# Kernel tuning notes

Measured on AMD Instinct MI355X. Metric: run time of the kernel, lower is better.

The kernel has to match this reference:

```python
import jax, jax.numpy as jnp
import numpy as np

B = 2048
INPUT_SIZE = 40960
HIDDEN = 256
ACTIVE = 30  # ~active features per chess position


def _multi_hot(key):
    idx = jax.random.randint(key, (B, ACTIVE), 0, INPUT_SIZE)
    oh = jnp.zeros((B, INPUT_SIZE), jnp.float32)
    return oh.at[jnp.arange(B)[:, None], idx].set(1.0)


def setup_inputs() -> dict:
    key = jax.random.key(0)
    kw, kb, ks, k1, k2, k3, k4 = jax.random.split(key, 7)
    white_onehot = _multi_hot(kw)
    black_onehot = _multi_hot(kb)
    stm = jax.random.randint(ks, (B, 1), 0, 2).astype(jnp.float32)
    # parameters (PyTorch Linear layout: weight [out, in])
    ft_w = jax.random.normal(k1, (HIDDEN, INPUT_SIZE), jnp.float32) * 0.02
    ft_b = jnp.zeros((HIDDEN,), jnp.float32)
    l1_w = jax.random.normal(k2, (32, HIDDEN * 2), jnp.float32) * 0.05
    l1_b = jnp.zeros((32,), jnp.float32)
    l2_w = jax.random.normal(k3, (32, 32), jnp.float32) * 0.1
    l2_b = jnp.zeros((32,), jnp.float32)
    l3_w = jax.random.normal(k4, (1, 32), jnp.float32) * 0.1
    l3_b = jnp.zeros((1,), jnp.float32)
    return dict(white_onehot=white_onehot, black_onehot=black_onehot, stm=stm,
                ft_w=ft_w, ft_b=ft_b, l1_w=l1_w, l1_b=l1_b,
                l2_w=l2_w, l2_b=l2_b, l3_w=l3_w, l3_b=l3_b)


def reference(white_onehot, black_onehot, stm,
              ft_w, ft_b, l1_w, l1_b, l2_w, l2_b, l3_w, l3_b):
    # feature transformer applied to dense one-hots (the wasteful dense GEMM)
    wh = jnp.clip(white_onehot @ ft_w.T + ft_b, 0.0, 1.0)  # [B, H]
    bh = jnp.clip(black_onehot @ ft_w.T + ft_b, 0.0, 1.0)  # [B, H]
    # side-to-move dependent perspective ordering
    hidden = jnp.where(stm.astype(bool),
                       jnp.concatenate([wh, bh], axis=-1),
                       jnp.concatenate([bh, wh], axis=-1))  # [B, 2H]
    x = jnp.clip(hidden @ l1_w.T + l1_b, 0.0, 1.0)
    x = jnp.clip(x @ l2_w.T + l2_b, 0.0, 1.0)
    return x @ l3_w.T + l3_b  # [B, 1]
```

## Files before the change

### kernel.cpp

```cpp
#include <hip/hip_runtime.h>

#define BATCH 2048
#define IN_SZ 40960
#define IN4   (IN_SZ / 4)
#define HID   256
#define LCAP  64

__global__ __launch_bounds__(256) void ft_transpose(const float* __restrict__ ftw,
                                                    float* __restrict__ ftT) {
    __shared__ float tile[32][33];
    const int tx = threadIdx.x;
    const int ty = threadIdx.y;
    const int bx = blockIdx.x;
    const int by = blockIdx.y;

    const int col = bx * 32 + tx;
#pragma unroll
    for (int j = 0; j < 32; j += 8) {
        const int row = by * 32 + ty + j;
        tile[ty + j][tx] = ftw[(size_t)row * IN_SZ + col];
    }
    __syncthreads();

    const int ocol = by * 32 + tx;
#pragma unroll
    for (int j = 0; j < 32; j += 8) {
        const int orow = bx * 32 + ty + j;
        ftT[(size_t)orow * HID + ocol] = tile[tx][ty + j];
    }
}

__global__ __launch_bounds__(256) void extract(const float* __restrict__ wo,
                                               const float* __restrict__ bo,
                                               int* __restrict__ cnt,
                                               int* __restrict__ lists)
{
    const int persp = blockIdx.y;
    const float4* __restrict__ src = (const float4*)(persp ? bo : wo);
    const int stride = gridDim.x * blockDim.x;
    for (int i = blockIdx.x * blockDim.x + threadIdx.x; i < BATCH * IN4; i += stride) {
        const float4 v = src[i];
        if (((v.x + v.y) + (v.z + v.w)) != 0.f) {
            const int row = i / IN4;
            const int f0  = (i - row * IN4) * 4;
            int* c = cnt + row * 2 + persp;
            int* l = lists + (row * 2 + persp) * LCAP;
            if (v.x != 0.f) l[atomicAdd(c, 1)] = f0;
            if (v.y != 0.f) l[atomicAdd(c, 1)] = f0 + 1;
            if (v.z != 0.f) l[atomicAdd(c, 1)] = f0 + 2;
            if (v.w != 0.f) l[atomicAdd(c, 1)] = f0 + 3;
        }
    }
}

__global__ __launch_bounds__(256) void ft_mlp(
    const int* __restrict__ cnt, const int* __restrict__ lists,
    const float* __restrict__ stm,
    const float* __restrict__ ftT, const float* __restrict__ ftb,
    const float* __restrict__ l1w, const float* __restrict__ l1b,
    const float* __restrict__ l2w, const float* __restrict__ l2b,
    const float* __restrict__ l3w, const float* __restrict__ l3b,
    float* __restrict__ out) {
    __shared__ int   sidx[2 * LCAP];
    __shared__ float hidden[2 * HID];
    __shared__ float x1[32], x2[32];

    const int b = blockIdx.x;
    const int t = threadIdx.x;

    if (t < 2 * LCAP) sidx[t] = lists[b * 2 * LCAP + t];
    __syncthreads();

    const int cw = cnt[b * 2 + 0];
    const int cb = cnt[b * 2 + 1];

    float accw = ftb[t];
    float accb = accw;
    for (int j = 0; j < cw; ++j) accw += ftT[(size_t)sidx[j] * HID + t];
    for (int j = 0; j < cb; ++j) accb += ftT[(size_t)sidx[LCAP + j] * HID + t];
    accw = fminf(fmaxf(accw, 0.f), 1.f);
    accb = fminf(fmaxf(accb, 0.f), 1.f);

    const bool s = (stm[b] != 0.f);
    hidden[t]       = s ? accw : accb;
    hidden[HID + t] = s ? accb : accw;
    __syncthreads();

    {
        const int o = t >> 3;
        const int part = t & 7;
        const float* w1 = l1w + o * (2 * HID);
        float sum = 0.f;
#pragma unroll 8
        for (int i = part; i < 2 * HID; i += 8)
            sum += hidden[i] * w1[i];
        sum += __shfl_xor(sum, 1);
        sum += __shfl_xor(sum, 2);
        sum += __shfl_xor(sum, 4);
        if (part == 0) x1[o] = fminf(fmaxf(sum + l1b[o], 0.f), 1.f);
    }
    __syncthreads();

    if (t < 32) {
        const float* w2 = l2w + t * 32;
        float sum = l2b[t];
#pragma unroll
        for (int i = 0; i < 32; ++i) sum += x1[i] * w2[i];
        x2[t] = fminf(fmaxf(sum, 0.f), 1.f);
    }
    __syncthreads();

    if (t == 0) {
        float sum = l3b[0];
#pragma unroll
        for (int i = 0; i < 32; ++i) sum += x2[i] * l3w[i];
        out[b] = sum;
    }
}

__global__ __launch_bounds__(256) void nnue_fused_fallback(
    const float* __restrict__ wo, const float* __restrict__ bo,
    const float* __restrict__ stm,
    const float* __restrict__ ftw, const float* __restrict__ ftb,
    const float* __restrict__ l1w, const float* __restrict__ l1b,
    const float* __restrict__ l2w, const float* __restrict__ l2b,
    const float* __restrict__ l3w, const float* __restrict__ l3b,
    float* __restrict__ out) {
    __shared__ int   idxw[LCAP], idxb[LCAP];
    __shared__ int   cntw, cntb;
    __shared__ float hidden[2 * HID];
    __shared__ float x1[32], x2[32];

    const int b = blockIdx.x;
    const int t = threadIdx.x;
    if (t == 0) { cntw = 0; cntb = 0; }
    __syncthreads();

    const float4* wrow = (const float4*)(wo + (size_t)b * IN_SZ);
    const float4* brow = (const float4*)(bo + (size_t)b * IN_SZ);
    for (int i = t; i < IN4; i += 256) {
        float4 v = wrow[i];
        float4 u = brow[i];
        if (((v.x + v.y) + (v.z + v.w)) != 0.f) {
            if (v.x != 0.f) idxw[atomicAdd(&cntw, 1)] = 4 * i;
            if (v.y != 0.f) idxw[atomicAdd(&cntw, 1)] = 4 * i + 1;
            if (v.z != 0.f) idxw[atomicAdd(&cntw, 1)] = 4 * i + 2;
            if (v.w != 0.f) idxw[atomicAdd(&cntw, 1)] = 4 * i + 3;
        }
        if (((u.x + u.y) + (u.z + u.w)) != 0.f) {
            if (u.x != 0.f) idxb[atomicAdd(&cntb, 1)] = 4 * i;
            if (u.y != 0.f) idxb[atomicAdd(&cntb, 1)] = 4 * i + 1;
            if (u.z != 0.f) idxb[atomicAdd(&cntb, 1)] = 4 * i + 2;
            if (u.w != 0.f) idxb[atomicAdd(&cntb, 1)] = 4 * i + 3;
        }
    }
    __syncthreads();

    float accw = ftb[t], accb = accw;
    for (int j = 0; j < cntw; ++j) accw += ftw[(size_t)t * IN_SZ + idxw[j]];
    for (int j = 0; j < cntb; ++j) accb += ftw[(size_t)t * IN_SZ + idxb[j]];
    accw = fminf(fmaxf(accw, 0.f), 1.f);
    accb = fminf(fmaxf(accb, 0.f), 1.f);

    const bool s = (stm[b] != 0.f);
    hidden[t]       = s ? accw : accb;
    hidden[HID + t] = s ? accb : accw;
    __syncthreads();

    {
        const int o = t >> 3, part = t & 7;
        const float* w1 = l1w + o * (2 * HID);
        float sum = 0.f;
        for (int i = part; i < 2 * HID; i += 8) sum += hidden[i] * w1[i];
        sum += __shfl_xor(sum, 1);
        sum += __shfl_xor(sum, 2);
        sum += __shfl_xor(sum, 4);
        if (part == 0) x1[o] = fminf(fmaxf(sum + l1b[o], 0.f), 1.f);
    }
    __syncthreads();
    if (t < 32) {
        float sum = l2b[t];
        for (int i = 0; i < 32; ++i) sum += x1[i] * l2w[t * 32 + i];
        x2[t] = fminf(fmaxf(sum, 0.f), 1.f);
    }
    __syncthreads();
    if (t == 0) {
        float sum = l3b[0];
        for (int i = 0; i < 32; ++i) sum += x2[i] * l3w[i];
        out[b] = sum;
    }
}

extern "C" void kernel_launch(void* const* d_in, const int* in_sizes, int n_in,
                              void* d_out, int out_size, void* d_ws, size_t ws_size,
                              hipStream_t stream) {
    const float* wo  = (const float*)d_in[0];
    const float* bo  = (const float*)d_in[1];
    const float* stm = (const float*)d_in[2];
    const float* ftw = (const float*)d_in[3];
    const float* ftb = (const float*)d_in[4];
    const float* l1w = (const float*)d_in[5];
    const float* l1b = (const float*)d_in[6];
    const float* l2w = (const float*)d_in[7];
    const float* l2b = (const float*)d_in[8];
    const float* l3w = (const float*)d_in[9];
    const float* l3b = (const float*)d_in[10];
    float* out = (float*)d_out;

    const size_t ftT_bytes  = (size_t)IN_SZ * HID * sizeof(float);
    const size_t cnt_off    = 44 * 1024 * 1024;
    const size_t cnt_bytes  = (size_t)BATCH * 2 * sizeof(int);
    const size_t list_off   = cnt_off + cnt_bytes;
    const size_t list_bytes = (size_t)BATCH * 2 * LCAP * sizeof(int);
    const size_t need       = list_off + list_bytes;

    if (ws_size >= need && ftT_bytes <= cnt_off) {
        float* ftT  = (float*)d_ws;
        int* cnt    = (int*)((char*)d_ws + cnt_off);
        int* lists  = (int*)((char*)d_ws + list_off);

        hipMemsetAsync(cnt, 0, cnt_bytes, stream);
        ft_transpose<<<dim3(IN_SZ / 32, HID / 32), dim3(32, 8), 0, stream>>>(ftw, ftT);
        extract<<<dim3(1024, 2), 256, 0, stream>>>(wo, bo, cnt, lists);
        ft_mlp<<<BATCH, 256, 0, stream>>>(cnt, lists, stm, ftT, ftb,
                                          l1w, l1b, l2w, l2b, l3w, l3b, out);
    } else {
        nnue_fused_fallback<<<BATCH, 256, 0, stream>>>(wo, bo, stm, ftw, ftb,
                                                       l1w, l1b, l2w, l2b, l3w, l3b, out);
    }
}
```

Before: 702.1 us.

## Fuse transpose, sparse extraction and MLP into one cooperative kernel

Replaces the memset plus three separate launches with a single cooperative kernel of 1024 blocks. Each block first transposes its share of the feature-transformer weights, then scans two batch rows' one-hot inputs and builds their index lists in shared memory, hits a grid-wide sync, and then runs the sparse accumulate and MLP for those rows. This removes launch gaps and the global count and list round-trip. In exchange it adds a grid barrier and needs 4 blocks per CU to be co-resident. Each block also handles two rows serially instead of one, which halves parallelism in the MLP phase.

Result: slower. 844.7 us (+20.3%).

```diff
diff --git a/kernel.cpp b/kernel.cpp
--- a/kernel.cpp
+++ b/kernel.cpp
@@ -1,120 +1,145 @@
 #include <hip/hip_runtime.h>
-
-#define BATCH 2048
-#define IN_SZ 40960
-#define IN4   (IN_SZ / 4)
-#define HID   256
-#define LCAP  64
-
-__global__ __launch_bounds__(256) void ft_transpose(const float* __restrict__ ftw,
-                                                    float* __restrict__ ftT) {
-    __shared__ float tile[32][33];
-    const int tx = threadIdx.x;
-    const int ty = threadIdx.y;
-    const int bx = blockIdx.x;
-    const int by = blockIdx.y;
-
-    const int col = bx * 32 + tx;
-#pragma unroll
-    for (int j = 0; j < 32; j += 8) {
-        const int row = by * 32 + ty + j;
-        tile[ty + j][tx] = ftw[(size_t)row * IN_SZ + col];
-    }
-    __syncthreads();
-
-    const int ocol = by * 32 + tx;
-#pragma unroll
-    for (int j = 0; j < 32; j += 8) {
-        const int orow = bx * 32 + ty + j;
-        ftT[(size_t)orow * HID + ocol] = tile[tx][ty + j];
-    }
-}
-
-__global__ __launch_bounds__(256) void extract(const float* __restrict__ wo,
-                                               const float* __restrict__ bo,
-                                               int* __restrict__ cnt,
-                                               int* __restrict__ lists)
-{
-    const int persp = blockIdx.y;
-    const float4* __restrict__ src = (const float4*)(persp ? bo : wo);
-    const int stride = gridDim.x * blockDim.x;
-    for (int i = blockIdx.x * blockDim.x + threadIdx.x; i < BATCH * IN4; i += stride) {
-        const float4 v = src[i];
-        if (((v.x + v.y) + (v.z + v.w)) != 0.f) {
-            const int row = i / IN4;
-            const int f0  = (i - row * IN4) * 4;
-            int* c = cnt + row * 2 + persp;
-            int* l = lists + (row * 2 + persp) * LCAP;
-            if (v.x != 0.f) l[atomicAdd(c, 1)] = f0;
-            if (v.y != 0.f) l[atomicAdd(c, 1)] = f0 + 1;
-            if (v.z != 0.f) l[atomicAdd(c, 1)] = f0 + 2;
-            if (v.w != 0.f) l[atomicAdd(c, 1)] = f0 + 3;
-        }
-    }
-}
-
-__global__ __launch_bounds__(256) void ft_mlp(
-    const int* __restrict__ cnt, const int* __restrict__ lists,
+#include <hip/hip_cooperative_groups.h>
+
+namespace cg = cooperative_groups;
+
+#define BATCH   2048
+#define IN_SZ   40960
+#define IN4     (IN_SZ / 4)
+#define HID     256
+#define LCAP    64
+#define NB      1024
+#define ROWS_PB (BATCH / NB)
+#define NTILES  ((IN_SZ / 32) * (HID / 32))
+
+__global__ __launch_bounds__(256, 4) void nnue_one(
+    const float* __restrict__ wo, const float* __restrict__ bo,
     const float* __restrict__ stm,
-    const float* __restrict__ ftT, const float* __restrict__ ftb,
+    const float* __restrict__ ftw, const float* __restrict__ ftb,
     const float* __restrict__ l1w, const float* __restrict__ l1b,
     const float* __restrict__ l2w, const float* __restrict__ l2b,
     const float* __restrict__ l3w, const float* __restrict__ l3b,
-    float* __restrict__ out) {
-    __shared__ int   sidx[2 * LCAP];
+    float* __restrict__ ftT, float* __restrict__ out)
+{
+    __shared__ float tile[32][33];
+    __shared__ int   idx[ROWS_PB][2][LCAP];
+    __shared__ int   cnt[ROWS_PB][2];
     __shared__ float hidden[2 * HID];
     __shared__ float x1[32], x2[32];
 
-    const int b = blockIdx.x;
-    const int t = threadIdx.x;
-
-    if (t < 2 * LCAP) sidx[t] = lists[b * 2 * LCAP + t];
-    __syncthreads();
-
-    const int cw = cnt[b * 2 + 0];
-    const int cb = cnt[b * 2 + 1];
-
-    float accw = ftb[t];
-    float accb = accw;
-    for (int j = 0; j < cw; ++j) accw += ftT[(size_t)sidx[j] * HID + t];
-    for (int j = 0; j < cb; ++j) accb += ftT[(size_t)sidx[LCAP + j] * HID + t];
-    accw = fminf(fmaxf(accw, 0.f), 1.f);
-    accb = fminf(fmaxf(accb, 0.f), 1.f);
-
-    const bool s = (stm[b] != 0.f);
-    hidden[t]       = s ? accw : accb;
-    hidden[HID + t] = s ? accb : accw;
-    __syncthreads();
+    const int t   = threadIdx.x;
+    const int blk = blockIdx.x;
+
+    if (t < ROWS_PB * 2) ((int*)cnt)[t] = 0;
 
     {
-        const int o = t >> 3;
-        const int part = t & 7;
-        const float* w1 = l1w + o * (2 * HID);
-        float sum = 0.f;
+        const int tx = t & 31;
+        const int ty = t >> 5;
+        for (int tid = blk; tid < NTILES; tid += NB) {
+            const int bx = tid >> 3;
+            const int by = tid & 7;
+            __syncthreads();
+#pragma unroll
+            for (int j = 0; j < 32; j += 8)
+                tile[ty + j][tx] = ftw[(size_t)(by * 32 + ty + j) * IN_SZ + bx * 32 + tx];
+            __syncthreads();
+#pragma unroll
+            for (int j = 0; j < 32; j += 8)
+                ftT[(size_t)(bx * 32 + ty + j) * HID + by * 32 + tx] = tile[tx][ty + j];
+        }
+    }
+    __syncthreads();
+
+    {
+        const int row0 = blk * ROWS_PB;
+        const float4* __restrict__ w0 = (const float4*)(wo + (size_t)row0 * IN_SZ);
+        const float4* __restrict__ b0 = (const float4*)(bo + (size_t)row0 * IN_SZ);
+        const float4* __restrict__ w1 = (const float4*)(wo + (size_t)(row0 + 1) * IN_SZ);
+        const float4* __restrict__ b1 = (const float4*)(bo + (size_t)(row0 + 1) * IN_SZ);
+
+        for (int i = t; i < IN4; i += 256) {
+            const float4 a0 = w0[i];
+            const float4 a1 = b0[i];
+            const float4 a2 = w1[i];
+            const float4 a3 = b1[i];
+            const int f0 = 4 * i;
+            if (((a0.x + a0.y) + (a0.z + a0.w)) != 0.f) {
+                if (a0.x != 0.f) idx[0][0][atomicAdd(&cnt[0][0], 1)] = f0;
+                if (a0.y != 0.f) idx[0][0][atomicAdd(&cnt[0][0], 1)] = f0 + 1;
+                if (a0.z != 0.f) idx[0][0][atomicAdd(&cnt[0][0], 1)] = f0 + 2;
+                if (a0.w != 0.f) idx[0][0][atomicAdd(&cnt[0][0], 1)] = f0 + 3;
+            }
+            if (((a1.x + a1.y) + (a1.z + a1.w)) != 0.f) {
+                if (a1.x != 0.f) idx[0][1][atomicAdd(&cnt[0][1], 1)] = f0;
+                if (a1.y != 0.f) idx[0][1][atomicAdd(&cnt[0][1], 1)] = f0 + 1;
+                if (a1.z != 0.f) idx[0][1][atomicAdd(&cnt[0][1], 1)] = f0 + 2;
+                if (a1.w != 0.f) idx[0][1][atomicAdd(&cnt[0][1], 1)] = f0 + 3;
+            }
+            if (((a2.x + a2.y) + (a2.z + a2.w)) != 0.f) {
+                if (a2.x != 0.f) idx[1][0][atomicAdd(&cnt[1][0], 1)] = f0;
+                if (a2.y != 0.f) idx[1][0][atomicAdd(&cnt[1][0], 1)] = f0 + 1;
+                if (a2.z != 0.f) idx[1][0][atomicAdd(&cnt[1][0], 1)] = f0 + 2;
+                if (a2.w != 0.f) idx[1][0][atomicAdd(&cnt[1][0], 1)] = f0 + 3;
+            }
+            if (((a3.x + a3.y) + (a3.z + a3.w)) != 0.f) {
+                if (a3.x != 0.f) idx[1][1][atomicAdd(&cnt[1][1], 1)] = f0;
+                if (a3.y != 0.f) idx[1][1][atomicAdd(&cnt[1][1], 1)] = f0 + 1;
+                if (a3.z != 0.f) idx[1][1][atomicAdd(&cnt[1][1], 1)] = f0 + 2;
+                if (a3.w != 0.f) idx[1][1][atomicAdd(&cnt[1][1], 1)] = f0 + 3;
+            }
+        }
+    }
+
+    cg::this_grid().sync();
+
+    for (int r = 0; r < ROWS_PB; ++r) {
+        const int row = blk * ROWS_PB + r;
+        const int cw = cnt[r][0];
+        const int cb = cnt[r][1];
+
+        float accw = ftb[t];
+        float accb = accw;
+        for (int j = 0; j < cw; ++j) accw += ftT[(size_t)idx[r][0][j] * HID + t];
+        for (int j = 0; j < cb; ++j) accb += ftT[(size_t)idx[r][1][j] * HID + t];
+        accw = fminf(fmaxf(accw, 0.f), 1.f);
+        accb = fminf(fmaxf(accb, 0.f), 1.f);
+
+        const bool s = (stm[row] != 0.f);
+        hidden[t]       = s ? accw : accb;
+        hidden[HID + t] = s ? accb : accw;
+        __syncthreads();
+
+        {
+            const int o = t >> 3;
+            const int part = t & 7;
+            const float* w1p = l1w + o * (2 * HID);
+            float sum = 0.f;
 #pragma unroll 8
-        for (int i = part; i < 2 * HID; i += 8)
-            sum += hidden[i] * w1[i];
-        sum += __shfl_xor(sum, 1);
-        sum += __shfl_xor(sum, 2);
-        sum += __shfl_xor(sum, 4);
-        if (part == 0) x1[o] = fminf(fmaxf(sum + l1b[o], 0.f), 1.f);
-    }
-    __syncthreads();
-
-    if (t < 32) {
-        const float* w2 = l2w + t * 32;
-        float sum = l2b[t];
-#pragma unroll
-        for (int i = 0; i < 32; ++i) sum += x1[i] * w2[i];
-        x2[t] = fminf(fmaxf(sum, 0.f), 1.f);
-    }
-    __syncthreads();
-
-    if (t == 0) {
-        float sum = l3b[0];
-#pragma unroll
-        for (int i = 0; i < 32; ++i) sum += x2[i] * l3w[i];
-        out[b] = sum;
+            for (int i = part; i < 2 * HID; i += 8)
+                sum += hidden[i] * w1p[i];
+            sum += __shfl_xor(sum, 1);
+            sum += __shfl_xor(sum, 2);
+            sum += __shfl_xor(sum, 4);
+            if (part == 0) x1[o] = fminf(fmaxf(sum + l1b[o], 0.f), 1.f);
+        }
+        __syncthreads();
+
+        if (t < 32) {
+            const float* w2 = l2w + t * 32;
+            float sum = l2b[t];
+#pragma unroll
+            for (int i = 0; i < 32; ++i) sum += x1[i] * w2[i];
+            x2[t] = fminf(fmaxf(sum, 0.f), 1.f);
+        }
+        __syncthreads();
+
+        if (t == 0) {
+            float sum = l3b[0];
+#pragma unroll
+            for (int i = 0; i < 32; ++i) sum += x2[i] * l3w[i];
+            out[row] = sum;
+        }
+        __syncthreads();
     }
 }
 
@@ -169,9 +194,9 @@
 
     {
         const int o = t >> 3, part = t & 7;
-        const float* w1 = l1w + o * (2 * HID);
+        const float* w1p = l1w + o * (2 * HID);
         float sum = 0.f;
-        for (int i = part; i < 2 * HID; i += 8) sum += hidden[i] * w1[i];
+        for (int i = part; i < 2 * HID; i += 8) sum += hidden[i] * w1p[i];
         sum += __shfl_xor(sum, 1);
         sum += __shfl_xor(sum, 2);
         sum += __shfl_xor(sum, 4);
@@ -207,24 +232,18 @@
     const float* l3b = (const float*)d_in[10];
     float* out = (float*)d_out;
 
-    const size_t ftT_bytes  = (size_t)IN_SZ * HID * sizeof(float);
-    const size_t cnt_off    = 44 * 1024 * 1024;
-    const size_t cnt_bytes  = (size_t)BATCH * 2 * sizeof(int);
-    const size_t list_off   = cnt_off + cnt_bytes;
-    const size_t list_bytes = (size_t)BATCH * 2 * LCAP * sizeof(int);
-    const size_t need       = list_off + list_bytes;
-
-    if (ws_size >= need && ftT_bytes <= cnt_off) {
-        float* ftT  = (float*)d_ws;
-        int* cnt    = (int*)((char*)d_ws + cnt_off);
-        int* lists  = (int*)((char*)d_ws + list_off);
-
-        hipMemsetAsync(cnt, 0, cnt_bytes, stream);
-        ft_transpose<<<dim3(IN_SZ / 32, HID / 32), dim3(32, 8), 0, stream>>>(ftw, ftT);
-        extract<<<dim3(1024, 2), 256, 0, stream>>>(wo, bo, cnt, lists);
-        ft_mlp<<<BATCH, 256, 0, stream>>>(cnt, lists, stm, ftT, ftb,
-                                          l1w, l1b, l2w, l2b, l3w, l3b, out);
-    } else {
+    const size_t ftT_bytes = (size_t)IN_SZ * HID * sizeof(float);
+    bool ok = false;
+    if (ws_size >= ftT_bytes) {
+        float* ftT = (float*)d_ws;
+        void* args[] = { (void*)&wo, (void*)&bo, (void*)&stm, (void*)&ftw, (void*)&ftb,
+                         (void*)&l1w, (void*)&l1b, (void*)&l2w, (void*)&l2b,
+                         (void*)&l3w, (void*)&l3b, (void*)&ftT, (void*)&out };
+        hipError_t rc = hipLaunchCooperativeKernel((const void*)nnue_one,
+                                                   dim3(NB), dim3(256), args, 0, stream);
+        ok = (rc == hipSuccess);
+    }
+    if (!ok) {
         nnue_fused_fallback<<<BATCH, 256, 0, stream>>>(wo, bo, stm, ftw, ftb,
                                                        l1w, l1b, l2w, l2b, l3w, l3b, out);
     }
```

## Fuse sparse index extraction into per-row FT+MLP kernel, drop memset and list buffers

Applied to the files above, without the earlier changes.

Merges the separate global-atomic extract kernel and the FT/MLP kernel into one per-batch-row kernel. Each block scans its own one-hot rows with integer OR tests, using a wave-wide __any skip and two loads in flight per perspective, and records indices through shared-memory atomics. This removes the memset, one launch, and the global list round trip. The trade-off is that each block streams 320 KB of input serially, which may give less memory parallelism than the grid-stride extract kernel. Integer nonzero tests treat -0.0 as nonzero, which does not matter for these inputs.

New measurement: 691.8 us. Within noise of the previous version (-1.5%).

```diff
diff --git a/kernel.cpp b/kernel.cpp
--- a/kernel.cpp
+++ b/kernel.cpp
@@ -30,54 +30,69 @@
     }
 }
 
-__global__ __launch_bounds__(256) void extract(const float* __restrict__ wo,
-                                               const float* __restrict__ bo,
-                                               int* __restrict__ cnt,
-                                               int* __restrict__ lists)
-{
-    const int persp = blockIdx.y;
-    const float4* __restrict__ src = (const float4*)(persp ? bo : wo);
-    const int stride = gridDim.x * blockDim.x;
-    for (int i = blockIdx.x * blockDim.x + threadIdx.x; i < BATCH * IN4; i += stride) {
-        const float4 v = src[i];
-        if (((v.x + v.y) + (v.z + v.w)) != 0.f) {
-            const int row = i / IN4;
-            const int f0  = (i - row * IN4) * 4;
-            int* c = cnt + row * 2 + persp;
-            int* l = lists + (row * 2 + persp) * LCAP;
-            if (v.x != 0.f) l[atomicAdd(c, 1)] = f0;
-            if (v.y != 0.f) l[atomicAdd(c, 1)] = f0 + 1;
-            if (v.z != 0.f) l[atomicAdd(c, 1)] = f0 + 2;
-            if (v.w != 0.f) l[atomicAdd(c, 1)] = f0 + 3;
-        }
-    }
-}
-
-__global__ __launch_bounds__(256) void ft_mlp(
-    const int* __restrict__ cnt, const int* __restrict__ lists,
+__global__ __launch_bounds__(256) void nnue_fused(
+    const float* __restrict__ wo, const float* __restrict__ bo,
     const float* __restrict__ stm,
-    const float* __restrict__ ftT, const float* __restrict__ ftb,
+    const float* __restrict__ ftT,
+    const float* __restrict__ ftb,
     const float* __restrict__ l1w, const float* __restrict__ l1b,
     const float* __restrict__ l2w, const float* __restrict__ l2b,
     const float* __restrict__ l3w, const float* __restrict__ l3b,
     float* __restrict__ out) {
-    __shared__ int   sidx[2 * LCAP];
+    __shared__ int   idxw[LCAP], idxb[LCAP];
+    __shared__ int   cntw, cntb;
     __shared__ float hidden[2 * HID];
     __shared__ float x1[32], x2[32];
 
     const int b = blockIdx.x;
     const int t = threadIdx.x;
 
-    if (t < 2 * LCAP) sidx[t] = lists[b * 2 * LCAP + t];
-    __syncthreads();
-
-    const int cw = cnt[b * 2 + 0];
-    const int cb = cnt[b * 2 + 1];
-
+    if (t == 0) { cntw = 0; cntb = 0; }
+    __syncthreads();
+
+    {
+        const uint4* __restrict__ wrow = (const uint4*)(wo + (size_t)b * IN_SZ);
+        const uint4* __restrict__ brow = (const uint4*)(bo + (size_t)b * IN_SZ);
+#pragma unroll 1
+        for (int i0 = t; i0 < IN4; i0 += 512) {
+            const int i1 = i0 + 256;
+            const uint4 w0 = wrow[i0];
+            const uint4 w1 = wrow[i1];
+            const uint4 b0 = brow[i0];
+            const uint4 b1 = brow[i1];
+            const unsigned mw0 = w0.x | w0.y | w0.z | w0.w;
+            const unsigned mw1 = w1.x | w1.y | w1.z | w1.w;
+            const unsigned mb0 = b0.x | b0.y | b0.z | b0.w;
+            const unsigned mb1 = b1.x | b1.y | b1.z | b1.w;
+            if (__any(mw0 | mw1)) {
+                if (w0.x) idxw[atomicAdd(&cntw, 1)] = 4 * i0;
+                if (w0.y) idxw[atomicAdd(&cntw, 1)] = 4 * i0 + 1;
+                if (w0.z) idxw[atomicAdd(&cntw, 1)] = 4 * i0 + 2;
+                if (w0.w) idxw[atomicAdd(&cntw, 1)] = 4 * i0 + 3;
+                if (w1.x) idxw[atomicAdd(&cntw, 1)] = 4 * i1;
+                if (w1.y) idxw[atomicAdd(&cntw, 1)] = 4 * i1 + 1;
+                if (w1.z) idxw[atomicAdd(&cntw, 1)] = 4 * i1 + 2;
+                if (w1.w) idxw[atomicAdd(&cntw, 1)] = 4 * i1 + 3;
+            }
+            if (__any(mb0 | mb1)) {
+                if (b0.x) idxb[atomicAdd(&cntb, 1)] = 4 * i0;
+                if (b0.y) idxb[atomicAdd(&cntb, 1)] = 4 * i0 + 1;
+                if (b0.z) idxb[atomicAdd(&cntb, 1)] = 4 * i0 + 2;
+                if (b0.w) idxb[atomicAdd(&cntb, 1)] = 4 * i0 + 3;
+                if (b1.x) idxb[atomicAdd(&cntb, 1)] = 4 * i1;
+                if (b1.y) idxb[atomicAdd(&cntb, 1)] = 4 * i1 + 1;
+                if (b1.z) idxb[atomicAdd(&cntb, 1)] = 4 * i1 + 2;
+                if (b1.w) idxb[atomicAdd(&cntb, 1)] = 4 * i1 + 3;
+            }
+        }
+    }
+    __syncthreads();
+
+    const int cw = cntw, cb = cntb;
     float accw = ftb[t];
     float accb = accw;
-    for (int j = 0; j < cw; ++j) accw += ftT[(size_t)sidx[j] * HID + t];
-    for (int j = 0; j < cb; ++j) accb += ftT[(size_t)sidx[LCAP + j] * HID + t];
+    for (int j = 0; j < cw; ++j) accw += ftT[(size_t)idxw[j] * HID + t];
+    for (int j = 0; j < cb; ++j) accb += ftT[(size_t)idxb[j] * HID + t];
     accw = fminf(fmaxf(accw, 0.f), 1.f);
     accb = fminf(fmaxf(accb, 0.f), 1.f);
 
@@ -89,11 +104,11 @@
     {
         const int o = t >> 3;
         const int part = t & 7;
-        const float* w1 = l1w + o * (2 * HID);
+        const float* w1p = l1w + o * (2 * HID);
         float sum = 0.f;
 #pragma unroll 8
         for (int i = part; i < 2 * HID; i += 8)
-            sum += hidden[i] * w1[i];
+            sum += hidden[i] * w1p[i];
         sum += __shfl_xor(sum, 1);
         sum += __shfl_xor(sum, 2);
         sum += __shfl_xor(sum, 4);
@@ -136,22 +151,22 @@
     if (t == 0) { cntw = 0; cntb = 0; }
     __syncthreads();
 
-    const float4* wrow = (const float4*)(wo + (size_t)b * IN_SZ);
-    const float4* brow = (const float4*)(bo + (size_t)b * IN_SZ);
+    const uint4* wrow = (const uint4*)(wo + (size_t)b * IN_SZ);
+    const uint4* brow = (const uint4*)(bo + (size_t)b * IN_SZ);
     for (int i = t; i < IN4; i += 256) {
-        float4 v = wrow[i];
-        float4 u = brow[i];
-        if (((v.x + v.y) + (v.z + v.w)) != 0.f) {
-            if (v.x != 0.f) idxw[atomicAdd(&cntw, 1)] = 4 * i;
-            if (v.y != 0.f) idxw[atomicAdd(&cntw, 1)] = 4 * i + 1;
-            if (v.z != 0.f) idxw[atomicAdd(&cntw, 1)] = 4 * i + 2;
-            if (v.w != 0.f) idxw[atomicAdd(&cntw, 1)] = 4 * i + 3;
+        uint4 v = wrow[i];
+        uint4 u = brow[i];
+        if (v.x | v.y | v.z | v.w) {
+            if (v.x) idxw[atomicAdd(&cntw, 1)] = 4 * i;
+            if (v.y) idxw[atomicAdd(&cntw, 1)] = 4 * i + 1;
+            if (v.z) idxw[atomicAdd(&cntw, 1)] = 4 * i + 2;
+            if (v.w) idxw[atomicAdd(&cntw, 1)] = 4 * i + 3;
         }
-        if (((u.x + u.y) + (u.z + u.w)) != 0.f) {
-            if (u.x != 0.f) idxb[atomicAdd(&cntb, 1)] = 4 * i;
-            if (u.y != 0.f) idxb[atomicAdd(&cntb, 1)] = 4 * i + 1;
-            if (u.z != 0.f) idxb[atomicAdd(&cntb, 1)] = 4 * i + 2;
-            if (u.w != 0.f) idxb[atomicAdd(&cntb, 1)] = 4 * i + 3;
+        if (u.x | u.y | u.z | u.w) {
+            if (u.x) idxb[atomicAdd(&cntb, 1)] = 4 * i;
+            if (u.y) idxb[atomicAdd(&cntb, 1)] = 4 * i + 1;
+            if (u.z) idxb[atomicAdd(&cntb, 1)] = 4 * i + 2;
+            if (u.w) idxb[atomicAdd(&cntb, 1)] = 4 * i + 3;
         }
     }
     __syncthreads();
@@ -169,9 +184,9 @@
 
     {
         const int o = t >> 3, part = t & 7;
-        const float* w1 = l1w + o * (2 * HID);
+        const float* w1p = l1w + o * (2 * HID);
         float sum = 0.f;
-        for (int i = part; i < 2 * HID; i += 8) sum += hidden[i] * w1[i];
+        for (int i = part; i < 2 * HID; i += 8) sum += hidden[i] * w1p[i];
         sum += __shfl_xor(sum, 1);
         sum += __shfl_xor(sum, 2);
         sum += __shfl_xor(sum, 4);
@@ -207,23 +222,12 @@
     const float* l3b = (const float*)d_in[10];
     float* out = (float*)d_out;
 
-    const size_t ftT_bytes  = (size_t)IN_SZ * HID * sizeof(float);
-    const size_t cnt_off    = 44 * 1024 * 1024;
-    const size_t cnt_bytes  = (size_t)BATCH * 2 * sizeof(int);
-    const size_t list_off   = cnt_off + cnt_bytes;
-    const size_t list_bytes = (size_t)BATCH * 2 * LCAP * sizeof(int);
-    const size_t need       = list_off + list_bytes;
-
-    if (ws_size >= need && ftT_bytes <= cnt_off) {
-        float* ftT  = (float*)d_ws;
-        int* cnt    = (int*)((char*)d_ws + cnt_off);
-        int* lists  = (int*)((char*)d_ws + list_off);
-
-        hipMemsetAsync(cnt, 0, cnt_bytes, stream);
+    const size_t ftT_bytes = (size_t)IN_SZ * HID * sizeof(float);
+    if (ws_size >= ftT_bytes) {
+        float* ftT = (float*)d_ws;
         ft_transpose<<<dim3(IN_SZ / 32, HID / 32), dim3(32, 8), 0, stream>>>(ftw, ftT);
-        extract<<<dim3(1024, 2), 256, 0, stream>>>(wo, bo, cnt, lists);
-        ft_mlp<<<BATCH, 256, 0, stream>>>(cnt, lists, stm, ftT, ftb,
-                                          l1w, l1b, l2w, l2b, l3w, l3b, out);
+        nnue_fused<<<BATCH, 256, 0, stream>>>(wo, bo, stm, ftT, ftb,
+                                              l1w, l1b, l2w, l2b, l3w, l3b, out);
     } else {
         nnue_fused_fallback<<<BATCH, 256, 0, stream>>>(wo, bo, stm, ftw, ftb,
                                                        l1w, l1b, l2w, l2b, l3w, l3b, out);
```
